# Optimization experiments

Hardware: AMD Instinct MI355X
Metric: run time of the kernel (lower is better)

The kernel has to match this reference:

```python
import jax, jax.numpy as jnp
import numpy as np

H = 4          # num_heads (= num_kv_heads, num_kv_groups = 1)
DK = 256       # head_k_dim
DV = 256       # head_v_dim
M = 256        # num_slots
GATE_NORM = 16.0
EPS = 1e-5


def _rmsnorm(x, w):
    var = jnp.mean(jnp.square(x), axis=-1, keepdims=True)
    return x * jax.lax.rsqrt(var + EPS) * w


def _swish(x):
    return x * jax.nn.sigmoid(x)


def setup_inputs() -> dict:
    key = jax.random.key(0)
    ks = jax.random.split(key, 8)
    B, T, D = 4, 2048, 1024
    scale = 2 ** (-2.5) * (2.0 / (D + D)) ** 0.5 * (3.0 ** 0.5) * 2  # ~xavier*gain magnitude
    return {
        "hidden_states": jax.random.normal(ks[0], (B, T, D), jnp.float32),
        "norm_weight": jnp.ones((D,), jnp.float32),
        "w_q": jax.random.normal(ks[1], (D, D), jnp.float32) * scale,
        "w_k": jax.random.normal(ks[2], (D, D), jnp.float32) * scale,
        "w_v": jax.random.normal(ks[3], (D, D), jnp.float32) * scale,
        "w_f": jax.random.normal(ks[4], (H * M, D), jnp.float32) * scale,
        "gnorm_weight": jnp.ones((D,), jnp.float32),
        "w_o": jax.random.normal(ks[5], (D, D), jnp.float32) * scale,
    }


def _gsa_scan(q, k, v, s, g):
    # all inputs time-major: q [T,B,H,DK], k [T,B,H,DK], v [T,B,H,DV],
    # s [T,B,H,M] (slot write strength), g [T,B,H,M] (log forget gate)
    B, Hh = q.shape[1], q.shape[2]
    Hk0 = jnp.zeros((B, Hh, DK, M), q.dtype)
    Hv0 = jnp.zeros((B, Hh, M, DV), q.dtype)

    def step(carry, xs):
        Hk, Hv = carry
        qt, kt, vt, st, gt = xs
        lam = jnp.exp(gt)                                       # [B,H,M]
        # pass 1: linear attn over slots (gate on value/slot dim)
        Hk = Hk * lam[:, :, None, :] + kt[..., :, None] * st[..., None, :]
        z = jnp.einsum('bhk,bhkm->bhm', qt, Hk)                 # slot logits
        p = jax.nn.softmax(z, axis=-1)                          # slot read weights
        # pass 2: linear attn from slots to values (gate on key/slot dim)
        Hv = Hv * lam[..., :, None] + st[..., :, None] * vt[..., None, :]
        ot = jnp.einsum('bhm,bhmv->bhv', p, Hv)
        return (Hk, Hv), ot

    _, o = jax.lax.scan(step, (Hk0, Hv0), (q, k, v, s, g))
    return o  # [T,B,H,DV]


def reference(hidden_states, norm_weight, w_q, w_k, w_v, w_f, gnorm_weight, w_o):
    B, T, D = hidden_states.shape
    h = _rmsnorm(hidden_states, norm_weight)                    # norm_first
    q = _swish(h @ w_q.T).reshape(B, T, H, DK)                  # swish feature map
    k = _swish(h @ w_k.T).reshape(B, T, H, DK)
    v = _swish(h @ w_v.T).reshape(B, T, H, DV)
    f = jax.nn.log_sigmoid(h @ w_f.T).reshape(B, T, H, M) / GATE_NORM
    s = 1.0 - jnp.exp(f)
    tm = lambda x: jnp.transpose(x, (1, 0, 2, 3))               # [B,T,H,*] -> [T,B,H,*]
    o = _gsa_scan(tm(q), tm(k), tm(v), tm(s), tm(f))            # [T,B,H,DV]
    o = jnp.transpose(o, (1, 0, 2, 3)).reshape(B, T, H * DV)
    # use_norm & no output gate: swish -> RMSNorm -> o_proj
    o = _swish(o)
    o = _rmsnorm(o, gnorm_weight)
    return o @ w_o.T
```

## Files before the change

kernel.cpp:

```cpp
#include <hip/hip_runtime.h>
#include <hip/hip_bf16.h>

typedef unsigned short u16;
typedef unsigned int u32;

using bf16x8 = __bf16 __attribute__((ext_vector_type(8)));
using s16x8  = short  __attribute__((ext_vector_type(8)));
using f32x4  = float  __attribute__((ext_vector_type(4)));

#define DEV static __device__ __forceinline__

constexpr int T_ = 2048, D_ = 1024;
constexpr int C_ = 64, NC_ = 32;
constexpr float EPS_ = 1e-5f;

DEV float bf2f(u16 u) { return __uint_as_float(((u32)u) << 16); }
DEV u16 f2bf(float f) {
  u32 u = __float_as_uint(f);
  return (u16)((u + 0x7fffu + ((u >> 16) & 1u)) >> 16);
}
DEV float swishf(float x) { return x / (1.f + __expf(-x)); }
DEV f32x4 zero4() { f32x4 z = {0.f, 0.f, 0.f, 0.f}; return z; }

DEV bf16x8 ld8(const u16* p, int ld, int r0, int k0, int lane) {
  return *(const bf16x8*)(p + (size_t)(r0 + (lane & 15)) * ld +
                          (size_t)(k0 + ((lane >> 4) << 3)));
}
DEV f32x4 MFMA(bf16x8 a, bf16x8 b, f32x4 c) {
  return __builtin_amdgcn_mfma_f32_16x16x32_bf16(a, b, c, 0, 0, 0);
}
DEV void gld_lds16(const void* g, void* l) {
  __builtin_amdgcn_global_load_lds(
      (const __attribute__((address_space(1))) unsigned int*)g,
      (__attribute__((address_space(3))) unsigned int*)l, 16, 0, 0);
}

__global__ __launch_bounds__(256) void k_cvt5(
    const float* __restrict__ s0, const float* __restrict__ s1,
    const float* __restrict__ s2, const float* __restrict__ s3,
    const float* __restrict__ s4, u16* __restrict__ d0, u16* __restrict__ d1,
    u16* __restrict__ d2, u16* __restrict__ d3, u16* __restrict__ d4) {
  const int wsel = blockIdx.x >> 10;
  const float* s = (wsel == 0) ? s0 : (wsel == 1) ? s1 : (wsel == 2) ? s2
                   : (wsel == 3) ? s3 : s4;
  u16* d = (wsel == 0) ? d0 : (wsel == 1) ? d1 : (wsel == 2) ? d2
           : (wsel == 3) ? d3 : d4;
  const int i = (blockIdx.x & 1023) * 256 + threadIdx.x;
  float4 v = ((const float4*)s)[i];
  uint2 o;
  o.x = (u32)f2bf(v.x) | ((u32)f2bf(v.y) << 16);
  o.y = (u32)f2bf(v.z) | ((u32)f2bf(v.w) << 16);
  ((uint2*)d)[i] = o;
}

__global__ __launch_bounds__(256) void k_rmsnorm(const float* __restrict__ x,
                                                 const float* __restrict__ w,
                                                 u16* __restrict__ h) {
  const int row = blockIdx.x, tid = threadIdx.x;
  float4 v = ((const float4*)(x + (size_t)row * D_))[tid];
  float ss = v.x * v.x + v.y * v.y + v.z * v.z + v.w * v.w;
#pragma unroll
  for (int d = 32; d >= 1; d >>= 1) ss += __shfl_xor(ss, d, 64);
  __shared__ float red[4];
  if ((tid & 63) == 0) red[tid >> 6] = ss;
  __syncthreads();
  float rs = rsqrtf((red[0] + red[1] + red[2] + red[3]) * (1.f / D_) + EPS_);
  float4 wv = ((const float4*)w)[tid];
  uint2 o;
  o.x = (u32)f2bf(v.x * rs * wv.x) | ((u32)f2bf(v.y * rs * wv.y) << 16);
  o.y = (u32)f2bf(v.z * rs * wv.z) | ((u32)f2bf(v.w * rs * wv.w) << 16);
  *(uint2*)(h + (size_t)row * D_ + tid * 4) = o;
}

__global__ __launch_bounds__(256) void k_swishnorm(const u16* __restrict__ x,
                                                   const float* __restrict__ w,
                                                   u16* __restrict__ o) {
  const int row = blockIdx.x, tid = threadIdx.x;
  uint2 pk = *(const uint2*)(x + (size_t)row * D_ + tid * 4);
  float v0 = swishf(bf2f((u16)(pk.x & 0xffff))), v1 = swishf(bf2f((u16)(pk.x >> 16)));
  float v2 = swishf(bf2f((u16)(pk.y & 0xffff))), v3 = swishf(bf2f((u16)(pk.y >> 16)));
  float ss = v0 * v0 + v1 * v1 + v2 * v2 + v3 * v3;
#pragma unroll
  for (int d = 32; d >= 1; d >>= 1) ss += __shfl_xor(ss, d, 64);
  __shared__ float red[4];
  if ((tid & 63) == 0) red[tid >> 6] = ss;
  __syncthreads();
  float rs = rsqrtf((red[0] + red[1] + red[2] + red[3]) * (1.f / D_) + EPS_);
  float4 wv = ((const float4*)w)[tid];
  uint2 ov;
  ov.x = (u32)f2bf(v0 * rs * wv.x) | ((u32)f2bf(v1 * rs * wv.y) << 16);
  ov.y = (u32)f2bf(v2 * rs * wv.z) | ((u32)f2bf(v3 * rs * wv.w) << 16);
  *(uint2*)(o + (size_t)row * D_ + tid * 4) = ov;
}

template <int MODE>
__global__ __launch_bounds__(256) void k_gemm(
    const u16* __restrict__ A, const u16* __restrict__ w0,
    const u16* __restrict__ w1, const u16* __restrict__ w2,
    const u16* __restrict__ w3, u16* __restrict__ oq, u16* __restrict__ okk,
    u16* __restrict__ ov, float* __restrict__ og, float* __restrict__ ofin) {
  __shared__ __align__(16) u16 As[128 * 32];
  __shared__ __align__(16) u16 Bs[128 * 32];
  const int z = blockIdx.z;
  const u16* W = (z == 0) ? w0 : (z == 1) ? w1 : (z == 2) ? w2 : w3;
  const int m0 = blockIdx.x * 128, n0 = blockIdx.y * 128;
  const int tid = threadIdx.x, lane = tid & 63, wvi = tid >> 6;
  const int wr = wvi >> 1, wc = wvi & 1;
  f32x4 acc[4][4];
#pragma unroll
  for (int i = 0; i < 4; i++)
#pragma unroll
    for (int j = 0; j < 4; j++) acc[i][j] = zero4();
  const int srow = tid >> 2, scb = (tid & 3) * 8;
  const u16* Ag = A + (size_t)(m0 + srow) * 1024 + scb;
  const u16* Wg = W + (size_t)(n0 + srow) * 1024 + scb;
  u16* AsW = As + (wvi * 16) * 32;
  u16* BsW = Bs + (wvi * 16) * 32;
  for (int kk = 0; kk < 1024; kk += 32) {
    gld_lds16(Ag + kk, AsW);
    gld_lds16(Ag + kk + 64 * 1024, AsW + 64 * 32);
    gld_lds16(Wg + kk, BsW);
    gld_lds16(Wg + kk + 64 * 1024, BsW + 64 * 32);
    __syncthreads();
    bf16x8 af[4], bfr[4];
#pragma unroll
    for (int i = 0; i < 4; i++) af[i] = ld8(As, 32, wr * 64 + 16 * i, 0, lane);
#pragma unroll
    for (int j = 0; j < 4; j++) bfr[j] = ld8(Bs, 32, wc * 64 + 16 * j, 0, lane);
#pragma unroll
    for (int i = 0; i < 4; i++)
#pragma unroll
      for (int j = 0; j < 4; j++) acc[i][j] = MFMA(af[i], bfr[j], acc[i][j]);
    __syncthreads();
  }
  const int q4 = lane >> 4, c15 = lane & 15;
#pragma unroll
  for (int i = 0; i < 4; i++)
#pragma unroll
    for (int j = 0; j < 4; j++)
#pragma unroll
      for (int r = 0; r < 4; r++) {
        int grow = m0 + wr * 64 + 16 * i + 4 * q4 + r;
        int gcol = n0 + wc * 64 + 16 * j + c15;
        size_t idx = (size_t)grow * 1024 + gcol;
        float val = acc[i][j][r];
        if (MODE == 1) {
          ofin[idx] = val;
        } else if (z < 3) {
          u16* o = (z == 0) ? oq : (z == 1) ? okk : ov;
          o[idx] = f2bf(swishf(val));
        } else {
          float g = (val >= 0.f) ? -log1pf(__expf(-val))
                                 : (val - log1pf(__expf(val)));
          og[idx] = g * (1.0f / 16.0f);
        }
      }
}

__global__ __launch_bounds__(256) void k_intra(
    const u16* __restrict__ kg, const u16* __restrict__ vg,
    const float* __restrict__ gg, u16* __restrict__ Sk, u16* __restrict__ Sv,
    float* __restrict__ Lam) {
  __shared__ __align__(16) u16 KV[256 * 72];
  __shared__ __align__(16) u16 Uh[128 * 72];
  __shared__ float LamH[128];
  const int c = blockIdx.x, p = blockIdx.y;
  const int b = p >> 2, hh = p & 3;
  const int R0 = b * T_ + c * C_, hb = hh * 256;
  const int tid = threadIdx.x, lane = tid & 63, wvi = tid >> 6;
  const int q4 = lane >> 4, c15 = lane & 15;
  const size_t scBase = ((size_t)p * NC_ + c) * (256 * 256);

  for (int t = 0; t < C_; t++)
    KV[tid * 72 + t] = kg[(size_t)(R0 + t) * D_ + hb + tid];
  __syncthreads();

  for (int mh = 0; mh < 2; mh++) {
    if (tid < 128) {
      int m = mh * 128 + tid;
      float ga = 0.f;
      for (int t = 0; t < C_; t++) {
        float gv = gg[(size_t)(R0 + t) * D_ + hb + m];
        ga += gv;
        Uh[tid * 72 + t] = f2bf((1.f - __expf(gv)) * __expf(-ga));
      }
      float lam = __expf(ga);
      LamH[tid] = lam;
      Lam[((size_t)p * NC_ + c) * 256 + m] = lam;
    }
    __syncthreads();
    for (int cb = 0; cb < 4; cb++) {
      f32x4 acc[2][4];
#pragma unroll
      for (int i = 0; i < 2; i++)
#pragma unroll
        for (int j = 0; j < 4; j++) acc[i][j] = zero4();
#pragma unroll
      for (int ks = 0; ks < 2; ks++) {
        bf16x8 af[2], bfr[4];
#pragma unroll
        for (int i = 0; i < 2; i++) af[i] = ld8(Uh, 72, 32 * wvi + 16 * i, 32 * ks, lane);
#pragma unroll
        for (int j = 0; j < 4; j++) bfr[j] = ld8(KV, 72, 64 * cb + 16 * j, 32 * ks, lane);
#pragma unroll
        for (int i = 0; i < 2; i++)
#pragma unroll
          for (int j = 0; j < 4; j++) acc[i][j] = MFMA(af[i], bfr[j], acc[i][j]);
      }
#pragma unroll
      for (int i = 0; i < 2; i++)
#pragma unroll
        for (int j = 0; j < 4; j++)
#pragma unroll
          for (int r = 0; r < 4; r++) {
            int ml = 32 * wvi + 16 * i + 4 * q4 + r;
            int dd = 64 * cb + 16 * j + c15;
            Sk[scBase + (size_t)(mh * 128 + ml) * 256 + dd] =
                f2bf(acc[i][j][r] * LamH[ml]);
          }
    }
    __syncthreads();
  }

  for (int t = 0; t < C_; t++)
    KV[tid * 72 + t] = vg[(size_t)(R0 + t) * D_ + hb + tid];
  __syncthreads();

  for (int mh = 0; mh < 2; mh++) {
    if (tid < 128) {
      int m = mh * 128 + tid;
      float ga = 0.f;
      for (int t = 0; t < C_; t++) {
        float gv = gg[(size_t)(R0 + t) * D_ + hb + m];
        ga += gv;
        Uh[tid * 72 + t] = f2bf((1.f - __expf(gv)) * __expf(-ga));
      }
      LamH[tid] = __expf(ga);
    }
    __syncthreads();
    for (int cb = 0; cb < 2; cb++) {
      f32x4 acc[4][4];
#pragma unroll
      for (int i = 0; i < 4; i++)
#pragma unroll
        for (int j = 0; j < 4; j++) acc[i][j] = zero4();
#pragma unroll
      for (int ks = 0; ks < 2; ks++) {
        bf16x8 af[4], bfr[4];
#pragma unroll
        for (int i = 0; i < 4; i++) af[i] = ld8(KV, 72, 64 * wvi + 16 * i, 32 * ks, lane);
#pragma unroll
        for (int j = 0; j < 4; j++) bfr[j] = ld8(Uh, 72, 64 * cb + 16 * j, 32 * ks, lane);
#pragma unroll
        for (int i = 0; i < 4; i++)
#pragma unroll
          for (int j = 0; j < 4; j++) acc[i][j] = MFMA(af[i], bfr[j], acc[i][j]);
      }
#pragma unroll
      for (int i = 0; i < 4; i++)
#pragma unroll
        for (int j = 0; j < 4; j++)
#pragma unroll
          for (int r = 0; r < 4; r++) {
            int vv = 64 * wvi + 16 * i + 4 * q4 + r;
            int ml = 64 * cb + 16 * j + c15;
            Sv[scBase + (size_t)vv * 256 + mh * 128 + ml] =
                f2bf(acc[i][j][r] * LamH[ml]);
          }
    }
    __syncthreads();
  }
}

__global__ __launch_bounds__(256) void k_scan(u16* __restrict__ Sk,
                                              u16* __restrict__ Sv,
                                              const float* __restrict__ Lam) {
  const int gid = blockIdx.x * 256 + threadIdx.x;
  const int st = gid >> 17;
  const int w = gid & 131071;
  const int p = w >> 13;
  const int r = (w >> 5) & 255;
  const int c0 = (w & 31) * 8;
  u16* S = st ? Sv : Sk;
  const size_t base = (size_t)p * NC_ * 65536 + (size_t)r * 256 + c0;
  const float* Lp = Lam + (size_t)p * NC_ * 256;
  float acc[8] = {0, 0, 0, 0, 0, 0, 0, 0};
  for (int c = 0; c < NC_; c++) {
    s16x8 in = *(const s16x8*)(S + base + (size_t)c * 65536);
    s16x8 ov;
#pragma unroll
    for (int j = 0; j < 8; j++) ov[j] = (short)f2bf(acc[j]);
    *(s16x8*)(S + base + (size_t)c * 65536) = ov;
    if (st == 0) {
      float lam = Lp[c * 256 + r];
#pragma unroll
      for (int j = 0; j < 8; j++) acc[j] = acc[j] * lam + bf2f((u16)in[j]);
    } else {
#pragma unroll
      for (int j = 0; j < 8; j++) {
        float lam = Lp[c * 256 + c0 + j];
        acc[j] = acc[j] * lam + bf2f((u16)in[j]);
      }
    }
  }
}

__global__ __launch_bounds__(256) void k_out(
    const u16* __restrict__ qg, const u16* __restrict__ kg,
    const u16* __restrict__ vg, const float* __restrict__ gg,
    const u16* __restrict__ Sk, const u16* __restrict__ Sv,
    u16* __restrict__ orw) {
  __shared__ __align__(16) char lds[61440];
  u16* As = (u16*)lds;
  u16* Ut = (u16*)(lds + 9216);
  float* Eh = (float*)(lds + 27648);
  u16* Pt = (u16*)(lds + 9216);
  u16* Vx = (u16*)(lds + 43008);

  const int c = blockIdx.x, p = blockIdx.y;
  const int b = p >> 2, hh = p & 3;
  const int R0 = b * T_ + c * C_, hb = hh * 256;
  const int tid = threadIdx.x, lane = tid & 63, wvi = tid >> 6;
  const int q4 = lane >> 4, c15 = lane & 15;
  const u16* qbase = qg + (size_t)R0 * D_ + hb;
  const u16* kbase = kg + (size_t)R0 * D_ + hb;
  const size_t scBase = ((size_t)p * NC_ + c) * 65536;
  const u16* SkC = Sk + scBase;
  const u16* SvC = Sv + scBase;

  {
    f32x4 acc[4];
#pragma unroll
    for (int n = 0; n < 4; n++) acc[n] = zero4();
#pragma unroll
    for (int ks = 0; ks < 8; ks++) {
      bf16x8 af = ld8(qbase, D_, 16 * wvi, 32 * ks, lane);
#pragma unroll
      for (int n = 0; n < 4; n++)
        acc[n] = MFMA(af, ld8(kbase, D_, 16 * n, 32 * ks, lane), acc[n]);
    }
#pragma unroll
    for (int n = 0; n < 4; n++)
#pragma unroll
      for (int r = 0; r < 4; r++) {
        int t = 16 * wvi + 4 * q4 + r, tau = 16 * n + c15;
        As[t * 72 + tau] = f2bf(tau <= t ? acc[n][r] : 0.f);
      }
  }
  __syncthreads();

  f32x4 zac[16], eRg[16];
#pragma unroll
  for (int mh = 0; mh < 2; mh++) {
    if (tid < 128) {
      int m = mh * 128 + tid;
      float ga = 0.f;
      for (int t = 0; t < C_; t++) {
        float gv = gg[(size_t)(R0 + t) * D_ + hb + m];
        ga += gv;
        Ut[tid * 72 + t] = f2bf((1.f - __expf(gv)) * __expf(-ga));
        Eh[t * 128 + tid] = __expf(ga);
      }
    }
    __syncthreads();
#pragma unroll
    for (int n = 0; n < 8; n++) zac[mh * 8 + n] = zero4();
#pragma unroll
    for (int ks = 0; ks < 2; ks++) {
      bf16x8 af = ld8(As, 72, 16 * wvi, 32 * ks, lane);
#pragma unroll
      for (int n = 0; n < 8; n++)
        zac[mh * 8 + n] = MFMA(af, ld8(Ut, 72, 16 * n, 32 * ks, lane), zac[mh * 8 + n]);
    }
#pragma unroll
    for (int ks = 0; ks < 8; ks++) {
      bf16x8 af = ld8(qbase, D_, 16 * wvi, 32 * ks, lane);
#pragma unroll
      for (int n = 0; n < 8; n++)
        zac[mh * 8 + n] = MFMA(
            af, ld8(SkC + (size_t)mh * 128 * 256, 256, 16 * n, 32 * ks, lane),
            zac[mh * 8 + n]);
    }
#pragma unroll
    for (int n = 0; n < 8; n++)
#pragma unroll
      for (int r = 0; r < 4; r++) {
        int t = 16 * wvi + 4 * q4 + r;
        float e = Eh[t * 128 + 16 * n + c15];
        eRg[mh * 8 + n][r] = e;
        zac[mh * 8 + n][r] *= e;
      }
    __syncthreads();
  }

#pragma unroll
  for (int r = 0; r < 4; r++) {
    float mx = -3.0e38f;
#pragma unroll
    for (int i = 0; i < 16; i++) mx = fmaxf(mx, zac[i][r]);
    mx = fmaxf(mx, __shfl_xor(mx, 1, 64));
    mx = fmaxf(mx, __shfl_xor(mx, 2, 64));
    mx = fmaxf(mx, __shfl_xor(mx, 4, 64));
    mx = fmaxf(mx, __shfl_xor(mx, 8, 64));
    float sm = 0.f;
#pragma unroll
    for (int i = 0; i < 16; i++) {
      float e = __expf(zac[i][r] - mx);
      zac[i][r] = e;
      sm += e;
    }
    sm += __shfl_xor(sm, 1, 64);
    sm += __shfl_xor(sm, 2, 64);
    sm += __shfl_xor(sm, 4, 64);
    sm += __shfl_xor(sm, 8, 64);
    float inv = 1.f / sm;
#pragma unroll
    for (int i = 0; i < 16; i++) zac[i][r] *= inv * eRg[i][r];
  }
#pragma unroll
  for (int i = 0; i < 16; i++)
#pragma unroll
    for (int r = 0; r < 4; r++) {
      int t = 16 * wvi + 4 * q4 + r;
      int m = (i >> 3) * 128 + 16 * (i & 7) + c15;
      Pt[t * 264 + m] = f2bf(zac[i][r]);
    }
  __syncthreads();

  {
    f32x4 wac[4];
#pragma unroll
    for (int n = 0; n < 4; n++) wac[n] = zero4();
    for (int mh = 0; mh < 2; mh++) {
      if (tid < 128) {
        int m = mh * 128 + tid;
        float ga = 0.f;
        for (int t = 0; t < C_; t++) {
          float gv = gg[(size_t)(R0 + t) * D_ + hb + m];
          ga += gv;
          Vx[tid * 72 + t] = f2bf((1.f - __expf(gv)) * __expf(-ga));
        }
      }
      __syncthreads();
#pragma unroll
      for (int ks = 0; ks < 4; ks++) {
        bf16x8 af = ld8(Pt, 264, 16 * wvi, mh * 128 + 32 * ks, lane);
        int mb = 32 * ks + (q4 << 3);
#pragma unroll
        for (int n = 0; n < 4; n++) {
          bf16x8 bfv;
#pragma unroll
          for (int j = 0; j < 8; j++)
            bfv[j] = __builtin_bit_cast(__bf16, (u16)Vx[(mb + j) * 72 + 16 * n + c15]);
          wac[n] = MFMA(af, bfv, wac[n]);
        }
      }
      __syncthreads();
    }
#pragma unroll
    for (int n = 0; n < 4; n++)
#pragma unroll
      for (int r = 0; r < 4; r++) {
        int t = 16 * wvi + 4 * q4 + r, tau = 16 * n + c15;
        As[t * 72 + tau] = f2bf(tau <= t ? wac[n][r] : 0.f);
      }
  }
  __syncthreads();

  for (int vh = 0; vh < 2; vh++) {
    if (tid < 128) {
      int v = vh * 128 + tid;
      for (int t = 0; t < C_; t++)
        Vx[tid * 72 + t] = vg[(size_t)(R0 + t) * D_ + hb + v];
    }
    __syncthreads();
    f32x4 oac[8];
#pragma unroll
    for (int n = 0; n < 8; n++) oac[n] = zero4();
#pragma unroll
    for (int ks = 0; ks < 8; ks++) {
      bf16x8 af = ld8(Pt, 264, 16 * wvi, 32 * ks, lane);
#pragma unroll
      for (int n = 0; n < 8; n++)
        oac[n] = MFMA(af, ld8(SvC + (size_t)vh * 128 * 256, 256, 16 * n, 32 * ks, lane), oac[n]);
    }
#pragma unroll
    for (int ks = 0; ks < 2; ks++) {
      bf16x8 af = ld8(As, 72, 16 * wvi, 32 * ks, lane);
#pragma unroll
      for (int n = 0; n < 8; n++)
        oac[n] = MFMA(af, ld8(Vx, 72, 16 * n, 32 * ks, lane), oac[n]);
    }
#pragma unroll
    for (int n = 0; n < 8; n++)
#pragma unroll
      for (int r = 0; r < 4; r++) {
        int t = 16 * wvi + 4 * q4 + r;
        int vc = vh * 128 + 16 * n + c15;
        orw[(size_t)(R0 + t) * D_ + hb + vc] = f2bf(oac[n][r]);
      }
    __syncthreads();
  }
}

extern "C" void kernel_launch(void* const* d_in, const int* in_sizes, int n_in,
                              void* d_out, int out_size, void* d_ws, size_t ws_size,
                              hipStream_t stream) {
  (void)in_sizes; (void)n_in; (void)out_size; (void)ws_size;
  const float* x   = (const float*)d_in[0];
  const float* nw  = (const float*)d_in[1];
  const float* wq  = (const float*)d_in[2];
  const float* wk  = (const float*)d_in[3];
  const float* wvp = (const float*)d_in[4];
  const float* wf  = (const float*)d_in[5];
  const float* gw  = (const float*)d_in[6];
  const float* wo  = (const float*)d_in[7];
  float* out = (float*)d_out;
  char* ws = (char*)d_ws;
  const size_t MB = 1024ull * 1024ull;
  u16*   hbuf = (u16*)(ws);
  u16*   qb   = (u16*)(ws + 16 * MB);
  u16*   kb   = (u16*)(ws + 32 * MB);
  u16*   vb   = (u16*)(ws + 48 * MB);
  float* gb   = (float*)(ws + 64 * MB);
  u16*   SkB  = (u16*)(ws + 96 * MB);
  u16*   SvB  = (u16*)(ws + 160 * MB);
  float* Lam  = (float*)(ws + 224 * MB);
  u16*   orw  = (u16*)(ws + 226 * MB);
  u16*   wqb  = (u16*)(ws + 242 * MB);
  u16*   wkb  = (u16*)(ws + 244 * MB);
  u16*   wvb  = (u16*)(ws + 246 * MB);
  u16*   wfb  = (u16*)(ws + 248 * MB);
  u16*   wob  = (u16*)(ws + 250 * MB);

  k_cvt5<<<dim3(5120), dim3(256), 0, stream>>>(wq, wk, wvp, wf, wo,
                                               wqb, wkb, wvb, wfb, wob);
  k_rmsnorm<<<dim3(8192), dim3(256), 0, stream>>>(x, nw, hbuf);
  k_gemm<0><<<dim3(64, 8, 4), dim3(256), 0, stream>>>(
      hbuf, wqb, wkb, wvb, wfb, qb, kb, vb, gb, (float*)nullptr);
  k_intra<<<dim3(NC_, 16), dim3(256), 0, stream>>>(kb, vb, gb, SkB, SvB, Lam);
  k_scan<<<dim3(1024), dim3(256), 0, stream>>>(SkB, SvB, Lam);
  k_out<<<dim3(NC_, 16), dim3(256), 0, stream>>>(qb, kb, vb, gb, SkB, SvB, orw);
  k_swishnorm<<<dim3(8192), dim3(256), 0, stream>>>(orw, gw, hbuf);
  k_gemm<1><<<dim3(64, 8, 1), dim3(256), 0, stream>>>(
      hbuf, wob, wob, wob, wob, (u16*)nullptr, (u16*)nullptr, (u16*)nullptr,
      (float*)nullptr, out);
}
```

Measured before the change: 544.4 us.

## Precompute chunk gate factors once; widen GEMM K-tile with swizzled LDS

Adds a k_gates kernel that computes the per-chunk decay cumsum, the U factors (stored transposed in bf16) and the cumulative exp values once, writing them in a chunk-major layout. k_intra and k_out then read these instead of recomputing the serial exp/cumsum loops over strided gate loads, which ran with only half the threads active. The projection GEMM now stages a 64-wide K tile per iteration with an XOR-swizzled LDS layout to cut LDS bank conflicts and halve the barrier count. In exchange it adds a kernel launch plus extra global traffic for U and E, and reuses the hbuf workspace for U.

Result: slower. 792.2 us (+45.5%).

```diff
diff --git a/kernel.cpp b/kernel.cpp
--- a/kernel.cpp
+++ b/kernel.cpp
@@ -25,6 +25,11 @@
 DEV bf16x8 ld8(const u16* p, int ld, int r0, int k0, int lane) {
   return *(const bf16x8*)(p + (size_t)(r0 + (lane & 15)) * ld +
                           (size_t)(k0 + ((lane >> 4) << 3)));
+}
+DEV bf16x8 ld8sw(const u16* p, int r0, int ks, int lane) {
+  int row = r0 + (lane & 15);
+  int kg = ks * 4 + (lane >> 4);
+  return *(const bf16x8*)(p + (size_t)row * 64 + ((kg ^ (row & 7)) << 3));
 }
 DEV f32x4 MFMA(bf16x8 a, bf16x8 b, f32x4 c) {
   return __builtin_amdgcn_mfma_f32_16x16x32_bf16(a, b, c, 0, 0, 0);
@@ -99,8 +104,8 @@
     const u16* __restrict__ w1, const u16* __restrict__ w2,
     const u16* __restrict__ w3, u16* __restrict__ oq, u16* __restrict__ okk,
     u16* __restrict__ ov, float* __restrict__ og, float* __restrict__ ofin) {
-  __shared__ __align__(16) u16 As[128 * 32];
-  __shared__ __align__(16) u16 Bs[128 * 32];
+  __shared__ __align__(16) u16 As[128 * 64];
+  __shared__ __align__(16) u16 Bs[128 * 64];
   const int z = blockIdx.z;
   const u16* W = (z == 0) ? w0 : (z == 1) ? w1 : (z == 2) ? w2 : w3;
   const int m0 = blockIdx.x * 128, n0 = blockIdx.y * 128;
@@ -111,26 +116,31 @@
   for (int i = 0; i < 4; i++)
 #pragma unroll
     for (int j = 0; j < 4; j++) acc[i][j] = zero4();
-  const int srow = tid >> 2, scb = (tid & 3) * 8;
-  const u16* Ag = A + (size_t)(m0 + srow) * 1024 + scb;
-  const u16* Wg = W + (size_t)(n0 + srow) * 1024 + scb;
-  u16* AsW = As + (wvi * 16) * 32;
-  u16* BsW = Bs + (wvi * 16) * 32;
-  for (int kk = 0; kk < 1024; kk += 32) {
-    gld_lds16(Ag + kk, AsW);
-    gld_lds16(Ag + kk + 64 * 1024, AsW + 64 * 32);
-    gld_lds16(Wg + kk, BsW);
-    gld_lds16(Wg + kk + 64 * 1024, BsW + 64 * 32);
+  const int srow = wvi * 8 + (lane >> 3);
+  const int sgrp = ((lane & 7) ^ ((lane >> 3) & 7)) * 8;
+  const u16* Ag = A + (size_t)(m0 + srow) * 1024 + sgrp;
+  const u16* Wg = W + (size_t)(n0 + srow) * 1024 + sgrp;
+  u16* AsW = As + (size_t)(wvi * 8) * 64;
+  u16* BsW = Bs + (size_t)(wvi * 8) * 64;
+  for (int kk = 0; kk < 1024; kk += 64) {
+#pragma unroll
+    for (int i = 0; i < 4; i++) {
+      gld_lds16(Ag + (size_t)(32 * i) * 1024 + kk, AsW + (size_t)(32 * i) * 64);
+      gld_lds16(Wg + (size_t)(32 * i) * 1024 + kk, BsW + (size_t)(32 * i) * 64);
+    }
     __syncthreads();
-    bf16x8 af[4], bfr[4];
-#pragma unroll
-    for (int i = 0; i < 4; i++) af[i] = ld8(As, 32, wr * 64 + 16 * i, 0, lane);
-#pragma unroll
-    for (int j = 0; j < 4; j++) bfr[j] = ld8(Bs, 32, wc * 64 + 16 * j, 0, lane);
-#pragma unroll
-    for (int i = 0; i < 4; i++)
-#pragma unroll
-      for (int j = 0; j < 4; j++) acc[i][j] = MFMA(af[i], bfr[j], acc[i][j]);
+#pragma unroll
+    for (int ks = 0; ks < 2; ks++) {
+      bf16x8 af[4], bfr[4];
+#pragma unroll
+      for (int i = 0; i < 4; i++) af[i] = ld8sw(As, wr * 64 + 16 * i, ks, lane);
+#pragma unroll
+      for (int j = 0; j < 4; j++) bfr[j] = ld8sw(Bs, wc * 64 + 16 * j, ks, lane);
+#pragma unroll
+      for (int i = 0; i < 4; i++)
+#pragma unroll
+        for (int j = 0; j < 4; j++) acc[i][j] = MFMA(af[i], bfr[j], acc[i][j]);
+    }
     __syncthreads();
   }
   const int q4 = lane >> 4, c15 = lane & 15;
@@ -142,133 +152,133 @@
       for (int r = 0; r < 4; r++) {
         int grow = m0 + wr * 64 + 16 * i + 4 * q4 + r;
         int gcol = n0 + wc * 64 + 16 * j + c15;
-        size_t idx = (size_t)grow * 1024 + gcol;
         float val = acc[i][j][r];
         if (MODE == 1) {
-          ofin[idx] = val;
+          ofin[(size_t)grow * 1024 + gcol] = val;
         } else if (z < 3) {
           u16* o = (z == 0) ? oq : (z == 1) ? okk : ov;
-          o[idx] = f2bf(swishf(val));
+          o[(size_t)grow * 1024 + gcol] = f2bf(swishf(val));
         } else {
           float g = (val >= 0.f) ? -log1pf(__expf(-val))
                                  : (val - log1pf(__expf(val)));
+          int bb = grow >> 11, tin = grow & 2047;
+          int cc = tin >> 6, tt = tin & 63;
+          int hh = gcol >> 8, mm = gcol & 255;
+          size_t idx = ((((size_t)(bb * 4 + hh) * NC_ + cc) * C_ + tt) << 8) + mm;
           og[idx] = g * (1.0f / 16.0f);
         }
       }
 }
 
+__global__ __launch_bounds__(256) void k_gates(float* __restrict__ g_inout,
+                                               u16* __restrict__ U_t,
+                                               float* __restrict__ Lam) {
+  const int c = blockIdx.x, p = blockIdx.y, tid = threadIdx.x;
+  const size_t base = ((size_t)p * NC_ + c) * (C_ * 256);
+  float ga = 0.f;
+  short ubuf[C_];
+#pragma unroll
+  for (int t = 0; t < C_; t++) {
+    float gv = g_inout[base + t * 256 + tid];
+    ga += gv;
+    float ea = __expf(ga);
+    ubuf[t] = (short)f2bf((1.f - __expf(gv)) / ea);
+    g_inout[base + t * 256 + tid] = ea;
+  }
+  Lam[((size_t)p * NC_ + c) * 256 + tid] = __expf(ga);
+  u16* up = U_t + ((size_t)p * NC_ + c) * (256 * C_) + (size_t)tid * C_;
+#pragma unroll
+  for (int i = 0; i < 8; i++) {
+    s16x8 w;
+#pragma unroll
+    for (int j = 0; j < 8; j++) w[j] = ubuf[i * 8 + j];
+    *(s16x8*)(up + i * 8) = w;
+  }
+}
+
 __global__ __launch_bounds__(256) void k_intra(
     const u16* __restrict__ kg, const u16* __restrict__ vg,
-    const float* __restrict__ gg, u16* __restrict__ Sk, u16* __restrict__ Sv,
-    float* __restrict__ Lam) {
+    const u16* __restrict__ U_t, const float* __restrict__ Lam,
+    u16* __restrict__ Sk, u16* __restrict__ Sv) {
   __shared__ __align__(16) u16 KV[256 * 72];
-  __shared__ __align__(16) u16 Uh[128 * 72];
-  __shared__ float LamH[128];
+  __shared__ float LamH[256];
   const int c = blockIdx.x, p = blockIdx.y;
   const int b = p >> 2, hh = p & 3;
   const int R0 = b * T_ + c * C_, hb = hh * 256;
   const int tid = threadIdx.x, lane = tid & 63, wvi = tid >> 6;
   const int q4 = lane >> 4, c15 = lane & 15;
-  const size_t scBase = ((size_t)p * NC_ + c) * (256 * 256);
-
+  const size_t chunk = (size_t)p * NC_ + c;
+  const u16* Uc = U_t + chunk * (256 * C_);
+  const size_t scBase = chunk * (256 * 256);
+
+  LamH[tid] = Lam[chunk * 256 + tid];
   for (int t = 0; t < C_; t++)
     KV[tid * 72 + t] = kg[(size_t)(R0 + t) * D_ + hb + tid];
   __syncthreads();
 
-  for (int mh = 0; mh < 2; mh++) {
-    if (tid < 128) {
-      int m = mh * 128 + tid;
-      float ga = 0.f;
-      for (int t = 0; t < C_; t++) {
-        float gv = gg[(size_t)(R0 + t) * D_ + hb + m];
-        ga += gv;
-        Uh[tid * 72 + t] = f2bf((1.f - __expf(gv)) * __expf(-ga));
-      }
-      float lam = __expf(ga);
-      LamH[tid] = lam;
-      Lam[((size_t)p * NC_ + c) * 256 + m] = lam;
-    }
-    __syncthreads();
-    for (int cb = 0; cb < 4; cb++) {
-      f32x4 acc[2][4];
-#pragma unroll
-      for (int i = 0; i < 2; i++)
-#pragma unroll
-        for (int j = 0; j < 4; j++) acc[i][j] = zero4();
-#pragma unroll
-      for (int ks = 0; ks < 2; ks++) {
-        bf16x8 af[2], bfr[4];
-#pragma unroll
-        for (int i = 0; i < 2; i++) af[i] = ld8(Uh, 72, 32 * wvi + 16 * i, 32 * ks, lane);
-#pragma unroll
-        for (int j = 0; j < 4; j++) bfr[j] = ld8(KV, 72, 64 * cb + 16 * j, 32 * ks, lane);
-#pragma unroll
-        for (int i = 0; i < 2; i++)
-#pragma unroll
-          for (int j = 0; j < 4; j++) acc[i][j] = MFMA(af[i], bfr[j], acc[i][j]);
-      }
-#pragma unroll
-      for (int i = 0; i < 2; i++)
-#pragma unroll
-        for (int j = 0; j < 4; j++)
-#pragma unroll
-          for (int r = 0; r < 4; r++) {
-            int ml = 32 * wvi + 16 * i + 4 * q4 + r;
-            int dd = 64 * cb + 16 * j + c15;
-            Sk[scBase + (size_t)(mh * 128 + ml) * 256 + dd] =
-                f2bf(acc[i][j][r] * LamH[ml]);
-          }
-    }
-    __syncthreads();
-  }
+  for (int cb = 0; cb < 4; cb++) {
+    f32x4 acc[4][4];
+#pragma unroll
+    for (int i = 0; i < 4; i++)
+#pragma unroll
+      for (int j = 0; j < 4; j++) acc[i][j] = zero4();
+#pragma unroll
+    for (int ks = 0; ks < 2; ks++) {
+      bf16x8 af[4], bfr[4];
+#pragma unroll
+      for (int i = 0; i < 4; i++) af[i] = ld8(Uc, C_, 64 * wvi + 16 * i, 32 * ks, lane);
+#pragma unroll
+      for (int j = 0; j < 4; j++) bfr[j] = ld8(KV, 72, 64 * cb + 16 * j, 32 * ks, lane);
+#pragma unroll
+      for (int i = 0; i < 4; i++)
+#pragma unroll
+        for (int j = 0; j < 4; j++) acc[i][j] = MFMA(af[i], bfr[j], acc[i][j]);
+    }
+#pragma unroll
+    for (int i = 0; i < 4; i++)
+#pragma unroll
+      for (int j = 0; j < 4; j++)
+#pragma unroll
+        for (int r = 0; r < 4; r++) {
+          int ml = 64 * wvi + 16 * i + 4 * q4 + r;
+          int dd = 64 * cb + 16 * j + c15;
+          Sk[scBase + (size_t)ml * 256 + dd] = f2bf(acc[i][j][r] * LamH[ml]);
+        }
+  }
+  __syncthreads();
 
   for (int t = 0; t < C_; t++)
     KV[tid * 72 + t] = vg[(size_t)(R0 + t) * D_ + hb + tid];
   __syncthreads();
 
-  for (int mh = 0; mh < 2; mh++) {
-    if (tid < 128) {
-      int m = mh * 128 + tid;
-      float ga = 0.f;
-      for (int t = 0; t < C_; t++) {
-        float gv = gg[(size_t)(R0 + t) * D_ + hb + m];
-        ga += gv;
-        Uh[tid * 72 + t] = f2bf((1.f - __expf(gv)) * __expf(-ga));
-      }
-      LamH[tid] = __expf(ga);
-    }
-    __syncthreads();
-    for (int cb = 0; cb < 2; cb++) {
-      f32x4 acc[4][4];
+  for (int cb = 0; cb < 4; cb++) {
+    f32x4 acc[4][4];
+#pragma unroll
+    for (int i = 0; i < 4; i++)
+#pragma unroll
+      for (int j = 0; j < 4; j++) acc[i][j] = zero4();
+#pragma unroll
+    for (int ks = 0; ks < 2; ks++) {
+      bf16x8 af[4], bfr[4];
+#pragma unroll
+      for (int i = 0; i < 4; i++) af[i] = ld8(KV, 72, 64 * wvi + 16 * i, 32 * ks, lane);
+#pragma unroll
+      for (int j = 0; j < 4; j++) bfr[j] = ld8(Uc, C_, 64 * cb + 16 * j, 32 * ks, lane);
 #pragma unroll
       for (int i = 0; i < 4; i++)
 #pragma unroll
-        for (int j = 0; j < 4; j++) acc[i][j] = zero4();
-#pragma unroll
-      for (int ks = 0; ks < 2; ks++) {
-        bf16x8 af[4], bfr[4];
-#pragma unroll
-        for (int i = 0; i < 4; i++) af[i] = ld8(KV, 72, 64 * wvi + 16 * i, 32 * ks, lane);
-#pragma unroll
-        for (int j = 0; j < 4; j++) bfr[j] = ld8(Uh, 72, 64 * cb + 16 * j, 32 * ks, lane);
-#pragma unroll
-        for (int i = 0; i < 4; i++)
-#pragma unroll
-          for (int j = 0; j < 4; j++) acc[i][j] = MFMA(af[i], bfr[j], acc[i][j]);
-      }
-#pragma unroll
-      for (int i = 0; i < 4; i++)
-#pragma unroll
-        for (int j = 0; j < 4; j++)
-#pragma unroll
-          for (int r = 0; r < 4; r++) {
-            int vv = 64 * wvi + 16 * i + 4 * q4 + r;
-            int ml = 64 * cb + 16 * j + c15;
-            Sv[scBase + (size_t)vv * 256 + mh * 128 + ml] =
-                f2bf(acc[i][j][r] * LamH[ml]);
-          }
-    }
-    __syncthreads();
+        for (int j = 0; j < 4; j++) acc[i][j] = MFMA(af[i], bfr[j], acc[i][j]);
+    }
+#pragma unroll
+    for (int i = 0; i < 4; i++)
+#pragma unroll
+      for (int j = 0; j < 4; j++)
+#pragma unroll
+        for (int r = 0; r < 4; r++) {
+          int vv = 64 * wvi + 16 * i + 4 * q4 + r;
+          int ml = 64 * cb + 16 * j + c15;
+          Sv[scBase + (size_t)vv * 256 + ml] = f2bf(acc[i][j][r] * LamH[ml]);
+        }
   }
 }
 
@@ -307,15 +317,14 @@
 
 __global__ __launch_bounds__(256) void k_out(
     const u16* __restrict__ qg, const u16* __restrict__ kg,
-    const u16* __restrict__ vg, const float* __restrict__ gg,
-    const u16* __restrict__ Sk, const u16* __restrict__ Sv,
-    u16* __restrict__ orw) {
+    const u16* __restrict__ vg, const u16* __restrict__ U_t,
+    const float* __restrict__ E, const u16* __restrict__ Sk,
+    const u16* __restrict__ Sv, u16* __restrict__ orw) {
   __shared__ __align__(16) char lds[61440];
   u16* As = (u16*)lds;
-  u16* Ut = (u16*)(lds + 9216);
-  float* Eh = (float*)(lds + 27648);
   u16* Pt = (u16*)(lds + 9216);
-  u16* Vx = (u16*)(lds + 43008);
+  u16* UnH = (u16*)(lds + 43008);
+  u16* VxH = (u16*)(lds + 43008);
 
   const int c = blockIdx.x, p = blockIdx.y;
   const int b = p >> 2, hh = p & 3;
@@ -324,9 +333,11 @@
   const int q4 = lane >> 4, c15 = lane & 15;
   const u16* qbase = qg + (size_t)R0 * D_ + hb;
   const u16* kbase = kg + (size_t)R0 * D_ + hb;
-  const size_t scBase = ((size_t)p * NC_ + c) * 65536;
-  const u16* SkC = Sk + scBase;
-  const u16* SvC = Sv + scBase;
+  const size_t chunk = (size_t)p * NC_ + c;
+  const u16* SkC = Sk + chunk * 65536;
+  const u16* SvC = Sv + chunk * 65536;
+  const u16* Uc = U_t + chunk * (256 * C_);
+  const float* Ec = E + chunk * (C_ * 256);
 
   {
     f32x4 acc[4];
@@ -349,20 +360,9 @@
   }
   __syncthreads();
 
-  f32x4 zac[16], eRg[16];
+  f32x4 zac[16];
 #pragma unroll
   for (int mh = 0; mh < 2; mh++) {
-    if (tid < 128) {
-      int m = mh * 128 + tid;
-      float ga = 0.f;
-      for (int t = 0; t < C_; t++) {
-        float gv = gg[(size_t)(R0 + t) * D_ + hb + m];
-        ga += gv;
-        Ut[tid * 72 + t] = f2bf((1.f - __expf(gv)) * __expf(-ga));
-        Eh[t * 128 + tid] = __expf(ga);
-      }
-    }
-    __syncthreads();
 #pragma unroll
     for (int n = 0; n < 8; n++) zac[mh * 8 + n] = zero4();
 #pragma unroll
@@ -370,7 +370,8 @@
       bf16x8 af = ld8(As, 72, 16 * wvi, 32 * ks, lane);
 #pragma unroll
       for (int n = 0; n < 8; n++)
-        zac[mh * 8 + n] = MFMA(af, ld8(Ut, 72, 16 * n, 32 * ks, lane), zac[mh * 8 + n]);
+        zac[mh * 8 + n] = MFMA(af, ld8(Uc, C_, mh * 128 + 16 * n, 32 * ks, lane),
+                               zac[mh * 8 + n]);
     }
 #pragma unroll
     for (int ks = 0; ks < 8; ks++) {
@@ -386,11 +387,8 @@
 #pragma unroll
       for (int r = 0; r < 4; r++) {
         int t = 16 * wvi + 4 * q4 + r;
-        float e = Eh[t * 128 + 16 * n + c15];
-        eRg[mh * 8 + n][r] = e;
-        zac[mh * 8 + n][r] *= e;
-      }
-    __syncthreads();
+        zac[mh * 8 + n][r] *= Ec[t * 256 + mh * 128 + 16 * n + c15];
+      }
   }
 
 #pragma unroll
@@ -414,8 +412,10 @@
     sm += __shfl_xor(sm, 4, 64);
     sm += __shfl_xor(sm, 8, 64);
     float inv = 1.f / sm;
-#pragma unroll
-    for (int i = 0; i < 16; i++) zac[i][r] *= inv * eRg[i][r];
+    int t = 16 * wvi + 4 * q4 + r;
+#pragma unroll
+    for (int i = 0; i < 16; i++)
+      zac[i][r] *= inv * Ec[t * 256 + (i >> 3) * 128 + 16 * (i & 7) + c15];
   }
 #pragma unroll
   for (int i = 0; i < 16; i++)
@@ -432,28 +432,24 @@
 #pragma unroll
     for (int n = 0; n < 4; n++) wac[n] = zero4();
     for (int mh = 0; mh < 2; mh++) {
-      if (tid < 128) {
-        int m = mh * 128 + tid;
-        float ga = 0.f;
-        for (int t = 0; t < C_; t++) {
-          float gv = gg[(size_t)(R0 + t) * D_ + hb + m];
-          ga += gv;
-          Vx[tid * 72 + t] = f2bf((1.f - __expf(gv)) * __expf(-ga));
+      {
+        int mloc = tid >> 1, th = tid & 1;
+        const u16* ur = Uc + (size_t)(mh * 128 + mloc) * C_ + th * 32;
+#pragma unroll
+        for (int tt = 0; tt < 4; tt++) {
+          s16x8 v = *(const s16x8*)(ur + tt * 8);
+#pragma unroll
+          for (int j = 0; j < 8; j++)
+            UnH[(th * 32 + tt * 8 + j) * 132 + mloc] = (u16)v[j];
         }
       }
       __syncthreads();
 #pragma unroll
       for (int ks = 0; ks < 4; ks++) {
         bf16x8 af = ld8(Pt, 264, 16 * wvi, mh * 128 + 32 * ks, lane);
-        int mb = 32 * ks + (q4 << 3);
-#pragma unroll
-        for (int n = 0; n < 4; n++) {
-          bf16x8 bfv;
-#pragma unroll
-          for (int j = 0; j < 8; j++)
-            bfv[j] = __builtin_bit_cast(__bf16, (u16)Vx[(mb + j) * 72 + 16 * n + c15]);
-          wac[n] = MFMA(af, bfv, wac[n]);
-        }
+#pragma unroll
+        for (int n = 0; n < 4; n++)
+          wac[n] = MFMA(af, ld8(UnH, 132, 16 * n, 32 * ks, lane), wac[n]);
       }
       __syncthreads();
     }
@@ -468,10 +464,13 @@
   __syncthreads();
 
   for (int vh = 0; vh < 2; vh++) {
-    if (tid < 128) {
-      int v = vh * 128 + tid;
-      for (int t = 0; t < C_; t++)
-        Vx[tid * 72 + t] = vg[(size_t)(R0 + t) * D_ + hb + v];
+    {
+      int vloc = tid >> 1, th = tid & 1;
+#pragma unroll 4
+      for (int tt = 0; tt < 32; tt++) {
+        int t = th * 32 + tt;
+        VxH[vloc * 72 + t] = vg[(size_t)(R0 + t) * D_ + hb + vh * 128 + vloc];
+      }
     }
     __syncthreads();
     f32x4 oac[8];
@@ -489,7 +488,7 @@
       bf16x8 af = ld8(As, 72, 16 * wvi, 32 * ks, lane);
 #pragma unroll
       for (int n = 0; n < 8; n++)
-        oac[n] = MFMA(af, ld8(Vx, 72, 16 * n, 32 * ks, lane), oac[n]);
+        oac[n] = MFMA(af, ld8(VxH, 72, 16 * n, 32 * ks, lane), oac[n]);
     }
 #pragma unroll
     for (int n = 0; n < 8; n++)
@@ -532,15 +531,17 @@
   u16*   wvb  = (u16*)(ws + 246 * MB);
   u16*   wfb  = (u16*)(ws + 248 * MB);
   u16*   wob  = (u16*)(ws + 250 * MB);
+  u16*   U_t  = hbuf;
 
   k_cvt5<<<dim3(5120), dim3(256), 0, stream>>>(wq, wk, wvp, wf, wo,
                                                wqb, wkb, wvb, wfb, wob);
   k_rmsnorm<<<dim3(8192), dim3(256), 0, stream>>>(x, nw, hbuf);
   k_gemm<0><<<dim3(64, 8, 4), dim3(256), 0, stream>>>(
       hbuf, wqb, wkb, wvb, wfb, qb, kb, vb, gb, (float*)nullptr);
-  k_intra<<<dim3(NC_, 16), dim3(256), 0, stream>>>(kb, vb, gb, SkB, SvB, Lam);
+  k_gates<<<dim3(NC_, 16), dim3(256), 0, stream>>>(gb, U_t, Lam);
+  k_intra<<<dim3(NC_, 16), dim3(256), 0, stream>>>(kb, vb, U_t, Lam, SkB, SvB);
   k_scan<<<dim3(1024), dim3(256), 0, stream>>>(SkB, SvB, Lam);
-  k_out<<<dim3(NC_, 16), dim3(256), 0, stream>>>(qb, kb, vb, gb, SkB, SvB, orw);
+  k_out<<<dim3(NC_, 16), dim3(256), 0, stream>>>(qb, kb, vb, U_t, gb, SkB, SvB, orw);
   k_swishnorm<<<dim3(8192), dim3(256), 0, stream>>>(orw, gw, hbuf);
   k_gemm<1><<<dim3(64, 8, 1), dim3(256), 0, stream>>>(
       hbuf, wob, wob, wob, wob, (u16*)nullptr, (u16*)nullptr, (u16*)nullptr,
```
